# Optimization experiments

Measured on AMD Instinct MI355X. Metric: run time of the kernel, lower is better.

## Reference

```python
import jax, jax.numpy as jnp
import numpy as np

B, S, E, N = 2, 2048, 768, 12
H = E // N

def setup_inputs() -> dict:
    key = jax.random.key(0)
    k1, k2, k3, k4, k5 = jax.random.split(key, 5)
    x = jax.random.normal(k1, (B, S, E), dtype=jnp.float32)
    Wqkv = jax.random.normal(k2, (E, 3 * E), dtype=jnp.float32) * (1.0 / np.sqrt(E))
    bqkv = jax.random.normal(k3, (3 * E,), dtype=jnp.float32) * 0.02
    Wproj = jax.random.normal(k4, (E, E), dtype=jnp.float32) * (1.0 / np.sqrt(E))
    bproj = jax.random.normal(k5, (E,), dtype=jnp.float32) * 0.02
    mask = jnp.tril(jnp.ones((S, S), dtype=jnp.int32))[None, None]  # (1,1,S,S) causal
    return {"mask": mask, "x": x, "Wqkv": Wqkv, "bqkv": bqkv, "Wproj": Wproj, "bproj": bproj}

def reference(mask, x, Wqkv, bqkv, Wproj, bproj):
    Bx, Sx, Ex = x.shape
    Hd = Ex // N
    qkv = x @ Wqkv + bqkv                       # (B,S,3E)
    q, k, v = jnp.split(qkv, 3, axis=-1)
    q = q.reshape(Bx, Sx, N, Hd).transpose(0, 2, 1, 3)  # (B,N,S,H)
    k = k.reshape(Bx, Sx, N, Hd).transpose(0, 2, 1, 3)
    v = v.reshape(Bx, Sx, N, Hd).transpose(0, 2, 1, 3)
    att = jnp.einsum('bnsh,bnth->bnst', q, k) / jnp.sqrt(jnp.float32(Hd))
    att = jnp.where(mask == 0, -jnp.inf, att)   # causal masked_fill
    p = jax.nn.softmax(att, axis=-1)            # dropout p=0.0 -> identity
    y = jnp.einsum('bnst,bnth->bnsh', p, v)     # (B,N,S,H)
    y = y.transpose(0, 2, 1, 3).reshape(Bx, Sx, Ex)
    return y @ Wproj + bproj
```

## Files before the change

### kernel.cpp

```cpp
#include <hip/hip_runtime.h>
#include <math.h>

#define S_LEN 2048
#define E_DIM 768
#define NHEAD 12
#define HDIM 64
#define BATCH 2
#define MROWS (BATCH * S_LEN)
#define KDIM E_DIM
#define NBN (BATCH * NHEAD)
#define NTASKS 768

typedef __attribute__((ext_vector_type(8))) short bf16x8;
typedef __attribute__((ext_vector_type(4))) float f32x4;

__device__ inline unsigned short f2bf(float f) {
    union { float f; unsigned u; } v; v.f = f;
    unsigned r = (v.u + 0x7FFFu + ((v.u >> 16) & 1u)) >> 16;
    return (unsigned short)r;
}

__global__ __launch_bounds__(256) void prep(
    const float* __restrict__ x, unsigned short* __restrict__ Xb,
    const float* __restrict__ Wqkv, unsigned short* __restrict__ WqkvT,
    const float* __restrict__ Wproj, unsigned short* __restrict__ WprojT)
{
    __shared__ float t[32][33];
    const int blk = blockIdx.x, tid = threadIdx.x;
    if (blk < 3072) {
        const int i = blk * 256 + tid;
        const float4 a = ((const float4*)x)[i];
        ushort4 o;
        o.x = f2bf(a.x); o.y = f2bf(a.y); o.z = f2bf(a.z); o.w = f2bf(a.w);
        ((ushort4*)Xb)[i] = o;
        return;
    }
    const float* W; unsigned short* WT; int N, bt;
    if (blk < 3072 + 1728) { bt = blk - 3072; N = 3 * E_DIM; W = Wqkv; WT = WqkvT; }
    else                   { bt = blk - 4800; N = E_DIM;     W = Wproj; WT = WprojT; }
    const int bx = bt % (N / 32), by = bt / (N / 32);
    const int k0 = by * 32, n0 = bx * 32;
    const int r = tid >> 3, c4 = (tid & 7) * 4;
    const float4 v = *(const float4*)&W[(size_t)(k0 + r) * N + n0 + c4];
    t[r][c4 + 0] = v.x; t[r][c4 + 1] = v.y; t[r][c4 + 2] = v.z; t[r][c4 + 3] = v.w;
    __syncthreads();
    ushort4 o;
    o.x = f2bf(t[c4 + 0][r]); o.y = f2bf(t[c4 + 1][r]);
    o.z = f2bf(t[c4 + 2][r]); o.w = f2bf(t[c4 + 3][r]);
    *(ushort4*)&WT[(size_t)(n0 + r) * KDIM + k0 + c4] = o;
}

template <int EPI>
__global__ __launch_bounds__(256, 5) void gemm64(
    const unsigned short* __restrict__ A, const unsigned short* __restrict__ BT,
    const float* __restrict__ bias, void* __restrict__ out0,
    void* __restrict__ out1, void* __restrict__ out2, int Nn)
{
    __shared__ unsigned short As[64 * 64];
    __shared__ unsigned short Bs[128 * 64];
    const int tid = threadIdx.x;
    const int lane = tid & 63;
    const int wid = tid >> 6;
    const int lr = lane & 15, lg = lane >> 4;
    const int wr = wid >> 1, wc = wid & 1;
    const int m0 = blockIdx.y * 64;
    const int n0 = blockIdx.x * 128;
    const int srow = lane >> 3, scol = (lane & 7) * 8;

    f32x4 acc[2][4];
    #pragma unroll
    for (int i = 0; i < 2; ++i)
        #pragma unroll
        for (int j = 0; j < 4; ++j) acc[i][j] = (f32x4){0.f, 0.f, 0.f, 0.f};

    for (int k0 = 0; k0 < KDIM; k0 += 64) {
        __syncthreads();
        #pragma unroll
        for (int c = 0; c < 2; ++c) {
            const int chunk = wid * 2 + c;
            const int row = chunk * 8 + srow;
            const unsigned short* ga = A + (size_t)(m0 + row) * KDIM + k0 + scol;
            __builtin_amdgcn_global_load_lds(
                (const __attribute__((address_space(1))) void*)ga,
                (__attribute__((address_space(3))) void*)&As[chunk * 512], 16, 0, 0);
        }
        #pragma unroll
        for (int c = 0; c < 4; ++c) {
            const int chunk = wid * 4 + c;
            const int row = chunk * 8 + srow;
            const unsigned short* gb = BT + (size_t)(n0 + row) * KDIM + k0 + scol;
            __builtin_amdgcn_global_load_lds(
                (const __attribute__((address_space(1))) void*)gb,
                (__attribute__((address_space(3))) void*)&Bs[chunk * 512], 16, 0, 0);
        }
        __syncthreads();

        #pragma unroll
        for (int kk = 0; kk < 2; ++kk) {
            bf16x8 af[2], bf[4];
            #pragma unroll
            for (int mt = 0; mt < 2; ++mt)
                af[mt] = *(const bf16x8*)&As[(wr * 32 + mt * 16 + lr) * 64 + kk * 32 + lg * 8];
            #pragma unroll
            for (int nt = 0; nt < 4; ++nt)
                bf[nt] = *(const bf16x8*)&Bs[(wc * 64 + nt * 16 + lr) * 64 + kk * 32 + lg * 8];
            #pragma unroll
            for (int mt = 0; mt < 2; ++mt)
                #pragma unroll
                for (int nt = 0; nt < 4; ++nt)
                    acc[mt][nt] = __builtin_amdgcn_mfma_f32_16x16x32_bf16(
                        af[mt], bf[nt], acc[mt][nt], 0, 0, 0);
        }
    }

    #pragma unroll
    for (int mt = 0; mt < 2; ++mt) {
        const int rowbase = m0 + wr * 32 + mt * 16 + lg * 4;
        #pragma unroll
        for (int nt = 0; nt < 4; ++nt) {
            const int col = n0 + wc * 64 + nt * 16 + lr;
            if (EPI == 0) {
                float* O = (float*)out0;
                const float bv = bias[col];
                #pragma unroll
                for (int r = 0; r < 4; ++r)
                    O[(size_t)(rowbase + r) * Nn + col] = acc[mt][nt][r] + bv;
            } else {
                const int which = col / E_DIM;
                const int rem = col % E_DIM;
                const int head = rem >> 6, h = rem & 63;
                const float bv = bias[col];
                if (which == 2) {
                    const int b = rowbase >> 11, s0 = rowbase & (S_LEN - 1);
                    unsigned short* VT = (unsigned short*)out2;
                    ushort4 pk;
                    pk.x = f2bf(acc[mt][nt][0] + bv);
                    pk.y = f2bf(acc[mt][nt][1] + bv);
                    pk.z = f2bf(acc[mt][nt][2] + bv);
                    pk.w = f2bf(acc[mt][nt][3] + bv);
                    *(ushort4*)&VT[((size_t)(b * NHEAD + head) * HDIM + h) * S_LEN + s0] = pk;
                } else {
                    unsigned short* dst = (which == 0) ? (unsigned short*)out0
                                                       : (unsigned short*)out1;
                    const float sc = (which == 0) ? 0.125f : 1.0f;
                    #pragma unroll
                    for (int r = 0; r < 4; ++r) {
                        const int m = rowbase + r;
                        const int b = m >> 11, s = m & (S_LEN - 1);
                        dst[(((size_t)(b * NHEAD + head) * S_LEN) + s) * HDIM + h] =
                            f2bf((acc[mt][nt][r] + bv) * sc);
                    }
                }
            }
        }
    }
}

__global__ __launch_bounds__(256) void attn_mfma(
    const unsigned short* __restrict__ Qb, const unsigned short* __restrict__ Kb,
    const unsigned short* __restrict__ VTb, unsigned short* __restrict__ Y,
    float* __restrict__ ws_o, float* __restrict__ ws_l)
{
    __shared__ unsigned short Ks[2][64 * 64];
    __shared__ unsigned short Vt[2][64 * 64];
    __shared__ unsigned short Ps[4 * 16 * 64];

    const int tid = threadIdx.x;
    const int lane = tid & 63;
    const int wid = tid >> 6;
    const int lr = lane & 15;
    const int lg = lane >> 4;

    const short one_bf = (short)0x3F80;
    bf16x8 onesB;
    #pragma unroll
    for (int j = 0; j < 8; ++j) onesB[j] = one_bf;

    const int sr0 = tid >> 3,        sc0 = (tid & 7) * 8;
    const int sr1 = 32 + (tid >> 3), sc1 = sc0;
    const int sw0 = sr0 * 64 + (sc0 ^ ((sr0 & 7) << 3));
    const int sw1 = sr1 * 64 + (sc1 ^ ((sr1 & 7) << 3));

    const int task = blockIdx.x;
    const int bn = task % NBN;
    const int rest = task / NBN;
    const int jj = rest & 15, half = rest >> 4;
    const int b = bn / NHEAD, n = bn % NHEAD;

    const unsigned short* Kg = Kb + (size_t)bn * S_LEN * HDIM;
    const unsigned short* Vg = VTb + (size_t)bn * HDIM * S_LEN;

    auto run_pass = [&](int qb, int t0, int t1, int mode) {
        const size_t qoff = ((size_t)bn * S_LEN + (qb * 64 + wid * 16 + lr)) * HDIM;
        const bf16x8 qA0 = *(const bf16x8*)(Qb + qoff + lg * 8);
        const bf16x8 qA1 = *(const bf16x8*)(Qb + qoff + 32 + lg * 8);

        f32x4 o[4];
        #pragma unroll
        for (int ht = 0; ht < 4; ++ht) o[ht] = (f32x4){0.f, 0.f, 0.f, 0.f};
        f32x4 lsum = (f32x4){0.f, 0.f, 0.f, 0.f};

        bf16x8 kreg0 = *(const bf16x8*)(Kg + ((size_t)t0 * 64 + sr0) * HDIM + sc0);
        bf16x8 kreg1 = *(const bf16x8*)(Kg + ((size_t)t0 * 64 + sr1) * HDIM + sc1);
        bf16x8 vreg0 = *(const bf16x8*)(Vg + (size_t)sr0 * S_LEN + t0 * 64 + sc0);
        bf16x8 vreg1 = *(const bf16x8*)(Vg + (size_t)sr1 * S_LEN + t0 * 64 + sc1);

        __syncthreads();
        *(bf16x8*)&Ks[0][sw0] = kreg0;  *(bf16x8*)&Ks[0][sw1] = kreg1;
        *(bf16x8*)&Vt[0][sw0] = vreg0;  *(bf16x8*)&Vt[0][sw1] = vreg1;
        if (t0 + 1 < t1) {
            kreg0 = *(const bf16x8*)(Kg + ((size_t)(t0 + 1) * 64 + sr0) * HDIM + sc0);
            kreg1 = *(const bf16x8*)(Kg + ((size_t)(t0 + 1) * 64 + sr1) * HDIM + sc1);
            vreg0 = *(const bf16x8*)(Vg + (size_t)sr0 * S_LEN + (t0 + 1) * 64 + sc0);
            vreg1 = *(const bf16x8*)(Vg + (size_t)sr1 * S_LEN + (t0 + 1) * 64 + sc1);
        }

        int cur = 0;
        for (int t = t0; t < t1; ++t) {
            __syncthreads();
            if (t + 1 < t1) {
                *(bf16x8*)&Ks[cur ^ 1][sw0] = kreg0;
                *(bf16x8*)&Ks[cur ^ 1][sw1] = kreg1;
                *(bf16x8*)&Vt[cur ^ 1][sw0] = vreg0;
                *(bf16x8*)&Vt[cur ^ 1][sw1] = vreg1;
                if (t + 2 < t1) {
                    kreg0 = *(const bf16x8*)(Kg + ((size_t)(t + 2) * 64 + sr0) * HDIM + sc0);
                    kreg1 = *(const bf16x8*)(Kg + ((size_t)(t + 2) * 64 + sr1) * HDIM + sc1);
                    vreg0 = *(const bf16x8*)(Vg + (size_t)sr0 * S_LEN + (t + 2) * 64 + sc0);
                    vreg1 = *(const bf16x8*)(Vg + (size_t)sr1 * S_LEN + (t + 2) * 64 + sc1);
                }
            }

            const unsigned short* Kc = Ks[cur];
            f32x4 s[4];
            __builtin_amdgcn_s_setprio(1);
            #pragma unroll
            for (int ct = 0; ct < 4; ++ct) {
                const int kr = ct * 16 + lr;
                const int xo = (kr & 7) << 3;
                const bf16x8 kb0 = *(const bf16x8*)&Kc[kr * 64 + ((lg * 8) ^ xo)];
                const bf16x8 kb1 = *(const bf16x8*)&Kc[kr * 64 + ((32 + lg * 8) ^ xo)];
                f32x4 a = (f32x4){0.f, 0.f, 0.f, 0.f};
                a = __builtin_amdgcn_mfma_f32_16x16x32_bf16(qA0, kb0, a, 0, 0, 0);
                a = __builtin_amdgcn_mfma_f32_16x16x32_bf16(qA1, kb1, a, 0, 0, 0);
                s[ct] = a;
            }
            __builtin_amdgcn_s_setprio(0);

            if (t == qb) {
                #pragma unroll
                for (int ct = 0; ct < 4; ++ct) {
                    const int col = t * 64 + ct * 16 + lr;
                    #pragma unroll
                    for (int r = 0; r < 4; ++r) {
                        const int qrow = qb * 64 + wid * 16 + lg * 4 + r;
                        if (col > qrow) s[ct][r] = -1e30f;
                    }
                }
            }

            unsigned short* Pw = Ps + wid * 1024;
            #pragma unroll
            for (int ct = 0; ct < 4; ++ct)
                #pragma unroll
                for (int r = 0; r < 4; ++r) {
                    const float p = __expf(s[ct][r] - 8.f);
                    const int prow = lg * 4 + r;
                    const int pcol = ct * 16 + lr;
                    Pw[prow * 64 + (pcol ^ ((prow & 7) << 3))] = f2bf(p);
                }

            const unsigned short* Vc = Vt[cur];
            const int pxo = (lr & 7) << 3;
            const bf16x8 pa0 = *(const bf16x8*)&Pw[lr * 64 + ((lg * 8) ^ pxo)];
            const bf16x8 pa1 = *(const bf16x8*)&Pw[lr * 64 + ((32 + lg * 8) ^ pxo)];
            __builtin_amdgcn_s_setprio(1);
            lsum = __builtin_amdgcn_mfma_f32_16x16x32_bf16(pa0, onesB, lsum, 0, 0, 0);
            lsum = __builtin_amdgcn_mfma_f32_16x16x32_bf16(pa1, onesB, lsum, 0, 0, 0);
            #pragma unroll
            for (int ht = 0; ht < 4; ++ht) {
                const int h = ht * 16 + lr;
                const int xo = (h & 7) << 3;
                const bf16x8 vb0 = *(const bf16x8*)&Vc[h * 64 + ((lg * 8) ^ xo)];
                const bf16x8 vb1 = *(const bf16x8*)&Vc[h * 64 + ((32 + lg * 8) ^ xo)];
                o[ht] = __builtin_amdgcn_mfma_f32_16x16x32_bf16(pa0, vb0, o[ht], 0, 0, 0);
                o[ht] = __builtin_amdgcn_mfma_f32_16x16x32_bf16(pa1, vb1, o[ht], 0, 0, 0);
            }
            __builtin_amdgcn_s_setprio(0);
            cur ^= 1;
        }

        if (mode == 2) {
            float invl[4];
            #pragma unroll
            for (int r = 0; r < 4; ++r) invl[r] = 1.f / lsum[r];
            #pragma unroll
            for (int r = 0; r < 4; ++r) {
                const int qrow = qb * 64 + wid * 16 + lg * 4 + r;
                unsigned short* yrow =
                    Y + ((size_t)(b * S_LEN + qrow)) * E_DIM + n * HDIM;
                #pragma unroll
                for (int ht = 0; ht < 4; ++ht)
                    yrow[ht * 16 + lr] = f2bf(o[ht][r] * invl[r]);
            }
        } else {
            const size_t m = (size_t)(bn * 16 + (qb - 16)) * 2 + mode;
            float* wo = ws_o + m * 4096;
            const int rowl = wid * 16 + lg * 4;
            #pragma unroll
            for (int ht = 0; ht < 4; ++ht)
                #pragma unroll
                for (int r = 0; r < 4; ++r)
                    wo[(rowl + r) * 64 + ht * 16 + lr] = o[ht][r];
            if (lr == 0) {
                float* wl = ws_l + m * 64;
                #pragma unroll
                for (int r = 0; r < 4; ++r) wl[rowl + r] = lsum[r];
            }
        }
    };

    if (half == 0) {
        run_pass(31 - jj, 0, 16, 0);
    } else {
        run_pass(31 - jj, 16, 32 - jj, 1);
        run_pass(jj, 0, jj + 1, 2);
    }
}

__global__ __launch_bounds__(256) void attn_merge(
    const float* __restrict__ ws_o, const float* __restrict__ ws_l,
    unsigned short* __restrict__ Y)
{
    const int m = blockIdx.x;
    const int bn = m / 16, qb = 16 + (m % 16);
    const int b = bn / NHEAD, n = bn % NHEAD;
    const int tid = threadIdx.x;
    const int r = tid >> 2, h0 = (tid & 3) * 16;

    const float* o0 = ws_o + ((size_t)m * 2 + 0) * 4096 + r * 64 + h0;
    const float* o1 = ws_o + ((size_t)m * 2 + 1) * 4096 + r * 64 + h0;
    const float l = ws_l[((size_t)m * 2 + 0) * 64 + r] +
                    ws_l[((size_t)m * 2 + 1) * 64 + r];
    const float inv = 1.f / l;
    unsigned short* yrow =
        Y + ((size_t)(b * S_LEN + qb * 64 + r)) * E_DIM + n * HDIM + h0;
    #pragma unroll
    for (int q = 0; q < 16; q += 4) {
        const float4 a = *(const float4*)(o0 + q);
        const float4 c = *(const float4*)(o1 + q);
        ushort4 pk;
        pk.x = f2bf((a.x + c.x) * inv); pk.y = f2bf((a.y + c.y) * inv);
        pk.z = f2bf((a.z + c.z) * inv); pk.w = f2bf((a.w + c.w) * inv);
        *(ushort4*)&yrow[q] = pk;
    }
}

extern "C" void kernel_launch(void* const* d_in, const int* in_sizes, int n_in,
                              void* d_out, int out_size, void* d_ws, size_t ws_size,
                              hipStream_t stream) {
    const float* x     = (const float*)d_in[1];
    const float* Wqkv  = (const float*)d_in[2];
    const float* bqkv  = (const float*)d_in[3];
    const float* Wproj = (const float*)d_in[4];
    const float* bproj = (const float*)d_in[5];
    float* out = (float*)d_out;

    const size_t per = (size_t)BATCH * NHEAD * S_LEN * HDIM;
    unsigned short* Xb     = (unsigned short*)d_ws;
    unsigned short* WqkvT  = Xb + (size_t)MROWS * E_DIM;
    unsigned short* WprojT = WqkvT + (size_t)3 * E_DIM * E_DIM;
    unsigned short* Qb     = WprojT + (size_t)E_DIM * E_DIM;
    unsigned short* Kb     = Qb + per;
    unsigned short* VTb    = Kb + per;
    unsigned short* Yb     = VTb + per;
    float*          ws_o   = (float*)(Yb + (size_t)MROWS * E_DIM);
    float*          ws_l   = ws_o + (size_t)384 * 2 * 4096;

    prep<<<5376, 256, 0, stream>>>(x, Xb, Wqkv, WqkvT, Wproj, WprojT);
    gemm64<1><<<dim3(3 * E_DIM / 128, MROWS / 64), 256, 0, stream>>>(
        Xb, WqkvT, bqkv, Qb, Kb, VTb, 3 * E_DIM);
    attn_mfma<<<NTASKS, 256, 0, stream>>>(Qb, Kb, VTb, Yb, ws_o, ws_l);
    attn_merge<<<384, 256, 0, stream>>>(ws_o, ws_l, Yb);
    gemm64<0><<<dim3(E_DIM / 128, MROWS / 64), 256, 0, stream>>>(
        Yb, WprojT, bproj, out, nullptr, nullptr, E_DIM);
}
```

Measured before the change: 89.15 us.

## Use direct global-to-LDS loads with pre-swizzled K/V and transposed score MFMA

The QKV GEMM epilogue now writes K and V^T in an XOR-swizzled layout, so the attention kernel can use global_load_lds to copy K/V tiles straight into shared memory without staging them through registers. The score MFMA operands are swapped so each lane holds a column of S^T. That lets P be written as packed ushort4 stores and lets the row sum come from scalar adds plus shuffles instead of extra MFMAs against a ones vector. The intent is to cut VGPR pressure, LDS write instructions and MFMA work. The cost is an implicit layout contract between kernels and a row-sum exchange through shared memory without a barrier.

```diff
diff --git a/kernel.cpp b/kernel.cpp
--- a/kernel.cpp
+++ b/kernel.cpp
@@ -132,13 +132,14 @@
                 const float bv = bias[col];
                 if (which == 2) {
                     const int b = rowbase >> 11, s0 = rowbase & (S_LEN - 1);
+                    const int scolv = (s0 & ~63) | ((s0 & 63) ^ ((h & 7) << 3));
                     unsigned short* VT = (unsigned short*)out2;
                     ushort4 pk;
                     pk.x = f2bf(acc[mt][nt][0] + bv);
                     pk.y = f2bf(acc[mt][nt][1] + bv);
                     pk.z = f2bf(acc[mt][nt][2] + bv);
                     pk.w = f2bf(acc[mt][nt][3] + bv);
-                    *(ushort4*)&VT[((size_t)(b * NHEAD + head) * HDIM + h) * S_LEN + s0] = pk;
+                    *(ushort4*)&VT[((size_t)(b * NHEAD + head) * HDIM + h) * S_LEN + scolv] = pk;
                 } else {
                     unsigned short* dst = (which == 0) ? (unsigned short*)out0
                                                        : (unsigned short*)out1;
@@ -147,7 +148,8 @@
                     for (int r = 0; r < 4; ++r) {
                         const int m = rowbase + r;
                         const int b = m >> 11, s = m & (S_LEN - 1);
-                        dst[(((size_t)(b * NHEAD + head) * S_LEN) + s) * HDIM + h] =
+                        const int hh = (which == 1) ? (h ^ ((s & 7) << 3)) : h;
+                        dst[(((size_t)(b * NHEAD + head) * S_LEN) + s) * HDIM + hh] =
                             f2bf((acc[mt][nt][r] + bv) * sc);
                     }
                 }
@@ -164,6 +166,7 @@
     __shared__ unsigned short Ks[2][64 * 64];
     __shared__ unsigned short Vt[2][64 * 64];
     __shared__ unsigned short Ps[4 * 16 * 64];
+    __shared__ float Ls[4][16];
 
     const int tid = threadIdx.x;
     const int lane = tid & 63;
@@ -171,16 +174,6 @@
     const int lr = lane & 15;
     const int lg = lane >> 4;
 
-    const short one_bf = (short)0x3F80;
-    bf16x8 onesB;
-    #pragma unroll
-    for (int j = 0; j < 8; ++j) onesB[j] = one_bf;
-
-    const int sr0 = tid >> 3,        sc0 = (tid & 7) * 8;
-    const int sr1 = 32 + (tid >> 3), sc1 = sc0;
-    const int sw0 = sr0 * 64 + (sc0 ^ ((sr0 & 7) << 3));
-    const int sw1 = sr1 * 64 + (sc1 ^ ((sr1 & 7) << 3));
-
     const int task = blockIdx.x;
     const int bn = task % NBN;
     const int rest = task / NBN;
@@ -192,42 +185,46 @@
 
     auto run_pass = [&](int qb, int t0, int t1, int mode) {
         const size_t qoff = ((size_t)bn * S_LEN + (qb * 64 + wid * 16 + lr)) * HDIM;
-        const bf16x8 qA0 = *(const bf16x8*)(Qb + qoff + lg * 8);
-        const bf16x8 qA1 = *(const bf16x8*)(Qb + qoff + 32 + lg * 8);
+        const bf16x8 qB0 = *(const bf16x8*)(Qb + qoff + lg * 8);
+        const bf16x8 qB1 = *(const bf16x8*)(Qb + qoff + 32 + lg * 8);
 
         f32x4 o[4];
         #pragma unroll
         for (int ht = 0; ht < 4; ++ht) o[ht] = (f32x4){0.f, 0.f, 0.f, 0.f};
-        f32x4 lsum = (f32x4){0.f, 0.f, 0.f, 0.f};
-
-        bf16x8 kreg0 = *(const bf16x8*)(Kg + ((size_t)t0 * 64 + sr0) * HDIM + sc0);
-        bf16x8 kreg1 = *(const bf16x8*)(Kg + ((size_t)t0 * 64 + sr1) * HDIM + sc1);
-        bf16x8 vreg0 = *(const bf16x8*)(Vg + (size_t)sr0 * S_LEN + t0 * 64 + sc0);
-        bf16x8 vreg1 = *(const bf16x8*)(Vg + (size_t)sr1 * S_LEN + t0 * 64 + sc1);
+        float lacc = 0.f;
 
         __syncthreads();
-        *(bf16x8*)&Ks[0][sw0] = kreg0;  *(bf16x8*)&Ks[0][sw1] = kreg1;
-        *(bf16x8*)&Vt[0][sw0] = vreg0;  *(bf16x8*)&Vt[0][sw1] = vreg1;
-        if (t0 + 1 < t1) {
-            kreg0 = *(const bf16x8*)(Kg + ((size_t)(t0 + 1) * 64 + sr0) * HDIM + sc0);
-            kreg1 = *(const bf16x8*)(Kg + ((size_t)(t0 + 1) * 64 + sr1) * HDIM + sc1);
-            vreg0 = *(const bf16x8*)(Vg + (size_t)sr0 * S_LEN + (t0 + 1) * 64 + sc0);
-            vreg1 = *(const bf16x8*)(Vg + (size_t)sr1 * S_LEN + (t0 + 1) * 64 + sc1);
+        #pragma unroll
+        for (int e = 0; e < 2; ++e) {
+            const int chunk = wid * 2 + e;
+            __builtin_amdgcn_global_load_lds(
+                (const __attribute__((address_space(1))) void*)
+                    (Kg + (size_t)t0 * 4096 + chunk * 512 + lane * 8),
+                (__attribute__((address_space(3))) void*)&Ks[0][chunk * 512], 16, 0, 0);
+            __builtin_amdgcn_global_load_lds(
+                (const __attribute__((address_space(1))) void*)
+                    (Vg + (size_t)(chunk * 8 + (lane >> 3)) * S_LEN + t0 * 64 + (lane & 7) * 8),
+                (__attribute__((address_space(3))) void*)&Vt[0][chunk * 512], 16, 0, 0);
         }
 
         int cur = 0;
         for (int t = t0; t < t1; ++t) {
             __syncthreads();
             if (t + 1 < t1) {
-                *(bf16x8*)&Ks[cur ^ 1][sw0] = kreg0;
-                *(bf16x8*)&Ks[cur ^ 1][sw1] = kreg1;
-                *(bf16x8*)&Vt[cur ^ 1][sw0] = vreg0;
-                *(bf16x8*)&Vt[cur ^ 1][sw1] = vreg1;
-                if (t + 2 < t1) {
-                    kreg0 = *(const bf16x8*)(Kg + ((size_t)(t + 2) * 64 + sr0) * HDIM + sc0);
-                    kreg1 = *(const bf16x8*)(Kg + ((size_t)(t + 2) * 64 + sr1) * HDIM + sc1);
-                    vreg0 = *(const bf16x8*)(Vg + (size_t)sr0 * S_LEN + (t + 2) * 64 + sc0);
-                    vreg1 = *(const bf16x8*)(Vg + (size_t)sr1 * S_LEN + (t + 2) * 64 + sc1);
+                #pragma unroll
+                for (int e = 0; e < 2; ++e) {
+                    const int chunk = wid * 2 + e;
+                    __builtin_amdgcn_global_load_lds(
+                        (const __attribute__((address_space(1))) void*)
+                            (Kg + (size_t)(t + 1) * 4096 + chunk * 512 + lane * 8),
+                        (__attribute__((address_space(3))) void*)&Ks[cur ^ 1][chunk * 512],
+                        16, 0, 0);
+                    __builtin_amdgcn_global_load_lds(
+                        (const __attribute__((address_space(1))) void*)
+                            (Vg + (size_t)(chunk * 8 + (lane >> 3)) * S_LEN + (t + 1) * 64
+                                + (lane & 7) * 8),
+                        (__attribute__((address_space(3))) void*)&Vt[cur ^ 1][chunk * 512],
+                        16, 0, 0);
                 }
             }
 
@@ -241,42 +238,42 @@
                 const bf16x8 kb0 = *(const bf16x8*)&Kc[kr * 64 + ((lg * 8) ^ xo)];
                 const bf16x8 kb1 = *(const bf16x8*)&Kc[kr * 64 + ((32 + lg * 8) ^ xo)];
                 f32x4 a = (f32x4){0.f, 0.f, 0.f, 0.f};
-                a = __builtin_amdgcn_mfma_f32_16x16x32_bf16(qA0, kb0, a, 0, 0, 0);
-                a = __builtin_amdgcn_mfma_f32_16x16x32_bf16(qA1, kb1, a, 0, 0, 0);
+                a = __builtin_amdgcn_mfma_f32_16x16x32_bf16(kb0, qB0, a, 0, 0, 0);
+                a = __builtin_amdgcn_mfma_f32_16x16x32_bf16(kb1, qB1, a, 0, 0, 0);
                 s[ct] = a;
             }
             __builtin_amdgcn_s_setprio(0);
 
             if (t == qb) {
+                const int q = qb * 64 + wid * 16 + lr;
                 #pragma unroll
                 for (int ct = 0; ct < 4; ++ct) {
-                    const int col = t * 64 + ct * 16 + lr;
                     #pragma unroll
                     for (int r = 0; r < 4; ++r) {
-                        const int qrow = qb * 64 + wid * 16 + lg * 4 + r;
-                        if (col > qrow) s[ct][r] = -1e30f;
+                        const int k = t * 64 + ct * 16 + lg * 4 + r;
+                        if (k > q) s[ct][r] = -1e30f;
                     }
                 }
             }
 
             unsigned short* Pw = Ps + wid * 1024;
-            #pragma unroll
-            for (int ct = 0; ct < 4; ++ct)
-                #pragma unroll
-                for (int r = 0; r < 4; ++r) {
-                    const float p = __expf(s[ct][r] - 8.f);
-                    const int prow = lg * 4 + r;
-                    const int pcol = ct * 16 + lr;
-                    Pw[prow * 64 + (pcol ^ ((prow & 7) << 3))] = f2bf(p);
-                }
+            const int pxo = (lr & 7) << 3;
+            #pragma unroll
+            for (int ct = 0; ct < 4; ++ct) {
+                const float p0 = __expf(s[ct][0] - 8.f);
+                const float p1 = __expf(s[ct][1] - 8.f);
+                const float p2 = __expf(s[ct][2] - 8.f);
+                const float p3 = __expf(s[ct][3] - 8.f);
+                lacc += (p0 + p1) + (p2 + p3);
+                ushort4 pk;
+                pk.x = f2bf(p0); pk.y = f2bf(p1); pk.z = f2bf(p2); pk.w = f2bf(p3);
+                *(ushort4*)&Pw[lr * 64 + ((ct * 16 + lg * 4) ^ pxo)] = pk;
+            }
 
             const unsigned short* Vc = Vt[cur];
-            const int pxo = (lr & 7) << 3;
             const bf16x8 pa0 = *(const bf16x8*)&Pw[lr * 64 + ((lg * 8) ^ pxo)];
             const bf16x8 pa1 = *(const bf16x8*)&Pw[lr * 64 + ((32 + lg * 8) ^ pxo)];
             __builtin_amdgcn_s_setprio(1);
-            lsum = __builtin_amdgcn_mfma_f32_16x16x32_bf16(pa0, onesB, lsum, 0, 0, 0);
-            lsum = __builtin_amdgcn_mfma_f32_16x16x32_bf16(pa1, onesB, lsum, 0, 0, 0);
             #pragma unroll
             for (int ht = 0; ht < 4; ++ht) {
                 const int h = ht * 16 + lr;
@@ -290,10 +287,13 @@
             cur ^= 1;
         }
 
+        lacc += __shfl_xor(lacc, 16, 64);
+        lacc += __shfl_xor(lacc, 32, 64);
+
         if (mode == 2) {
-            float invl[4];
-            #pragma unroll
-            for (int r = 0; r < 4; ++r) invl[r] = 1.f / lsum[r];
+            if (lg == 0) Ls[wid][lr] = lacc;
+            const float4 lv = *(const float4*)&Ls[wid][lg * 4];
+            const float invl[4] = {1.f / lv.x, 1.f / lv.y, 1.f / lv.z, 1.f / lv.w};
             #pragma unroll
             for (int r = 0; r < 4; ++r) {
                 const int qrow = qb * 64 + wid * 16 + lg * 4 + r;
@@ -312,11 +312,7 @@
                 #pragma unroll
                 for (int r = 0; r < 4; ++r)
                     wo[(rowl + r) * 64 + ht * 16 + lr] = o[ht][r];
-            if (lr == 0) {
-                float* wl = ws_l + m * 64;
-                #pragma unroll
-                for (int r = 0; r < 4; ++r) wl[rowl + r] = lsum[r];
-            }
+            if (lg == 0) ws_l[m * 64 + wid * 16 + lr] = lacc;
         }
     };
 
```

Measured after the change: 89.19 us. No clear change (+0.0%).
